# Performance work log

Measured on AMD Instinct MI355X. Metric: run time of the kernel, lower is better.

The kernel has to match this reference:

```python
import jax, jax.numpy as jnp
import numpy as np
import math

NG, NP, NC = 300, 100000, 80
ALPHA, BETA = 0.75, 1.0
K_MAX, K_MIN = 10, 1
EPS = 1e-7


def k_schedule(epoch, total_epochs):
    t = epoch / max(1, total_epochs - 1)
    K = int(round(K_MAX - (K_MAX - K_MIN) * t))
    return max(K_MIN, min(K_MAX, K))


def setup_inputs() -> dict:
    key = jax.random.key(0)
    k1, k2, k3 = jax.random.split(key, 3)
    preds = jax.random.normal(k1, (NP, 5 + NC), dtype=jnp.float32)
    gt_boxes = jax.random.uniform(k2, (NG, 4), dtype=jnp.float32)
    gt_classes = jax.random.randint(k3, (NG,), 0, NC, dtype=jnp.int32)
    return {"preds": preds, "gt_boxes": gt_boxes, "gt_classes": gt_classes,
            "epoch": 0, "total_epochs": 300}


def _cost_matrix(preds, gt_boxes, gt_classes):
    # preds: [Np, 5+C] (xywh, obj, cls_logits); gt_boxes: [Ng, 4] xyxy
    xc, yc, w, h = preds[:, 0], preds[:, 1], preds[:, 2], preds[:, 3]
    p = jnp.stack([xc - w / 2, yc - h / 2, xc + w / 2, yc + h / 2], axis=-1)  # [Np,4] xyxy
    g = gt_boxes  # [Ng,4]

    p_ = p[None, :, :]   # [1,Np,4]
    g_ = g[:, None, :]   # [Ng,1,4]

    # IoU  (bbox_iou with ci=pred, cj=gt)
    x1 = jnp.maximum(p_[..., 0], g_[..., 0])
    y1 = jnp.maximum(p_[..., 1], g_[..., 1])
    x2 = jnp.minimum(p_[..., 2], g_[..., 2])
    y2 = jnp.minimum(p_[..., 3], g_[..., 3])
    inter = jnp.clip(x2 - x1, 0) * jnp.clip(y2 - y1, 0)          # [Ng,Np]
    area_p = jnp.clip(p[:, 2] - p[:, 0], 0) * jnp.clip(p[:, 3] - p[:, 1], 0)   # [Np]
    area_g = jnp.clip(g[:, 2] - g[:, 0], 0) * jnp.clip(g[:, 3] - g[:, 1], 0)   # [Ng]
    union = area_p[None, :] + area_g[:, None] - inter + EPS
    iou = inter / union

    # center distance
    pcx = (p[:, 0] + p[:, 2]) / 2; pcy = (p[:, 1] + p[:, 3]) / 2   # [Np]
    gcx = (g[:, 0] + g[:, 2]) / 2; gcy = (g[:, 1] + g[:, 3]) / 2   # [Ng]
    center_dist2 = (pcx[None, :] - gcx[:, None]) ** 2 + (pcy[None, :] - gcy[:, None]) ** 2

    # enclosing box diagonal
    c_w = jnp.clip(jnp.maximum(p_[..., 2], g_[..., 2]) - jnp.minimum(p_[..., 0], g_[..., 0]), EPS)
    c_h = jnp.clip(jnp.maximum(p_[..., 3], g_[..., 3]) - jnp.minimum(p_[..., 1], g_[..., 1]), EPS)
    c2 = c_w ** 2 + c_h ** 2 + EPS

    # aspect-ratio term
    wp = jnp.clip(p[:, 2] - p[:, 0], EPS); hp = jnp.clip(p[:, 3] - p[:, 1], EPS)  # [Np]
    wg = jnp.clip(g[:, 2] - g[:, 0], EPS); hg = jnp.clip(g[:, 3] - g[:, 1], EPS)  # [Ng]
    v = (4.0 / math.pi ** 2) * (jnp.arctan(wg / hg)[:, None] - jnp.arctan(wp / hp)[None, :]) ** 2
    alpha_t = jax.lax.stop_gradient(v / ((1.0 - iou) + v + EPS))   # torch.no_grad block
    ciou = iou - center_dist2 / c2 - alpha_t * v                   # [Ng,Np] (= 1 - ciou_loss)

    # classification score for each pred at its gt's class
    cls_prob = jax.nn.sigmoid(preds[:, 5:])                        # [Np,C]
    cls_score = jnp.take(cls_prob, gt_classes, axis=1).T           # [Ng,Np]

    cost = ALPHA * (1.0 - cls_score) + BETA * (1.0 - jnp.clip(ciou, 0.0, 1.0))
    return cost


def reference(preds, gt_boxes, gt_classes, epoch, total_epochs):
    Ng, Np = gt_boxes.shape[0], preds.shape[0]
    Kt = min(k_schedule(epoch, total_epochs), Np)
    cost = _cost_matrix(preds, gt_boxes, gt_classes)               # [Ng,Np]
    _, topk_idx = jax.lax.top_k(-cost, Kt)                         # [Ng,Kt] smallest cost per gt
    gt_idx = jnp.broadcast_to(jnp.arange(Ng, dtype=topk_idx.dtype)[:, None], topk_idx.shape)
    assignments = jnp.stack([topk_idx.reshape(-1), gt_idx.reshape(-1)], axis=1)  # [Ng*Kt,2]
    return cost, assignments
```

## Files before the change

kernel.cpp:

```cpp
#include <hip/hip_runtime.h>
#include <math.h>

#define NG 300
#define NP 100000
#define NC 80
#define PRED_COLS 85
#define ALPHA_C 0.75f
#define BETA_C  1.0f
#define EPS_C   1e-7f
#define TPB 256
#define BCH 10
#define CHUNK (NP / BCH)
#define KCAP 10
#define NSLAB 20
#define GSLAB (NG / NSLAB)
#define CTILE 16
#define NCT (NC / CTILE)

__device__ __forceinline__ float fast_rcp(float x) {
    return __builtin_amdgcn_rcpf(x);
}

__global__ __launch_bounds__(TPB) void prep_kernel(
    const float* __restrict__ preds, float* __restrict__ probs,
    float4* __restrict__ bA, float4* __restrict__ bB)
{
    int p = blockIdx.x * TPB + threadIdx.x;
    if (p >= NP) return;
    if (blockIdx.y < NCT) {
        int c0 = blockIdx.y * CTILE;
        const float* row = preds + (size_t)p * PRED_COLS + 5 + c0;
#pragma unroll
        for (int j = 0; j < CTILE; ++j) {
            float l = row[j];
            probs[(size_t)(c0 + j) * NP + p] = fast_rcp(1.f + expf(-l));
        }
    } else {
        const float* row = preds + (size_t)p * PRED_COLS;
        float xc = row[0], yc = row[1], w = row[2], h = row[3];
        float px1 = xc - w * 0.5f, py1 = yc - h * 0.5f;
        float px2 = xc + w * 0.5f, py2 = yc + h * 0.5f;
        float4 a = {px1, py1, px2, py2};
        float4 b;
        b.x = fmaxf(px2 - px1, 0.f) * fmaxf(py2 - py1, 0.f);
        b.y = (px1 + px2) * 0.5f;
        b.z = (py1 + py2) * 0.5f;
        b.w = atanf(fmaxf(px2 - px1, EPS_C) / fmaxf(py2 - py1, EPS_C));
        bA[p] = a; bB[p] = b;
    }
}

template <bool USE_PACK>
__global__ __launch_bounds__(TPB) void cost_kernel(
    const float* __restrict__ preds, const float* __restrict__ gt_boxes,
    const int* __restrict__ gt_classes, float* __restrict__ cost,
    const float* __restrict__ probs,
    const float4* __restrict__ bA, const float4* __restrict__ bB)
{
    __shared__ float4 sbox[GSLAB];
    __shared__ float4 smisc[GSLAB];
    __shared__ int    scls[GSLAB];

    const int g0 = blockIdx.y * GSLAB;

    for (int i = threadIdx.x; i < GSLAB; i += TPB) {
        int g = g0 + i;
        float4 b = ((const float4*)gt_boxes)[g];
        float x1 = b.x, y1 = b.y, x2 = b.z, y2 = b.w;
        sbox[i] = b;
        float4 m;
        m.x = fmaxf(x2 - x1, 0.f) * fmaxf(y2 - y1, 0.f);
        m.y = (x1 + x2) * 0.5f;
        m.z = (y1 + y2) * 0.5f;
        m.w = atanf(fmaxf(x2 - x1, EPS_C) / fmaxf(y2 - y1, EPS_C));
        smisc[i] = m;
        scls[i] = gt_classes[g] * NP;
    }
    __syncthreads();

    int p = blockIdx.x * TPB + threadIdx.x;
    if (p >= NP) return;

    float px1, py1, px2, py2, areap, pcx, pcy, atp;
    if (USE_PACK) {
        float4 a = bA[p], b = bB[p];
        px1 = a.x; py1 = a.y; px2 = a.z; py2 = a.w;
        areap = b.x; pcx = b.y; pcy = b.z; atp = b.w;
    } else {
        const float* row = preds + (size_t)p * PRED_COLS;
        float xc = row[0], yc = row[1], w = row[2], h = row[3];
        px1 = xc - w * 0.5f; py1 = yc - h * 0.5f;
        px2 = xc + w * 0.5f; py2 = yc + h * 0.5f;
        areap = fmaxf(px2 - px1, 0.f) * fmaxf(py2 - py1, 0.f);
        pcx = (px1 + px2) * 0.5f; pcy = (py1 + py2) * 0.5f;
        atp = atanf(fmaxf(px2 - px1, EPS_C) / fmaxf(py2 - py1, EPS_C));
    }

    const float VC = (float)(4.0 / (M_PI * M_PI));
    float* out = cost + (size_t)g0 * NP + p;

#pragma unroll 5
    for (int i = 0; i < GSLAB; ++i) {
        float4 b = sbox[i];
        float4 m = smisc[i];
        float gx1 = b.x, gy1 = b.y, gx2 = b.z, gy2 = b.w;
        float xx1 = fmaxf(px1, gx1), yy1 = fmaxf(py1, gy1);
        float xx2 = fminf(px2, gx2), yy2 = fminf(py2, gy2);
        float inter = fmaxf(xx2 - xx1, 0.f) * fmaxf(yy2 - yy1, 0.f);
        float uni = areap + m.x - inter + EPS_C;
        float iou = inter * fast_rcp(uni);
        float dx = pcx - m.y, dy = pcy - m.z;
        float cd2 = dx * dx + dy * dy;
        float cw = fmaxf(fmaxf(px2, gx2) - fminf(px1, gx1), EPS_C);
        float ch = fmaxf(fmaxf(py2, gy2) - fminf(py1, gy1), EPS_C);
        float c2 = cw * cw + ch * ch + EPS_C;
        float dat = m.w - atp;
        float v = VC * dat * dat;
        float alpha_t = v * fast_rcp(1.f - iou + v + EPS_C);
        float ciou = iou - cd2 * fast_rcp(c2) - alpha_t * v;

        float prob = probs[(size_t)scls[i] + p];
        float cst = ALPHA_C * (1.f - prob) +
                    BETA_C * (1.f - fminf(fmaxf(ciou, 0.f), 1.f));
        out[(size_t)i * NP] = cst;
    }
}

__device__ __forceinline__ void wave_lexmin(float& v, int& i) {
#pragma unroll
    for (int off = 32; off >= 1; off >>= 1) {
        float ov = __shfl_xor(v, off);
        int   oi = __shfl_xor(i, off);
        if (ov < v || (ov == v && oi < i)) { v = ov; i = oi; }
    }
}

__global__ __launch_bounds__(TPB) void topk_partial(
    const float* __restrict__ cost, float* __restrict__ lc, int* __restrict__ li)
{
    int g  = blockIdx.x / BCH;
    int ch = blockIdx.x % BCH;
    const float4* b4 = (const float4*)(cost + (size_t)g * NP + (size_t)ch * CHUNK);
    const int NV = CHUNK / 4;

    const int lane = threadIdx.x & 63;
    const int wid  = threadIdx.x >> 6;

    float lmin = INFINITY;
    for (int i = threadIdx.x; i < NV; i += TPB) {
        float4 v = b4[i];
        lmin = fminf(lmin, fminf(fminf(v.x, v.y), fminf(v.z, v.w)));
    }
    float thr;
    {
        float v = lmin;
        float last = INFINITY;
#pragma unroll
        for (int k = 0; k < KCAP; ++k) {
            float wv = v; int wi = lane;
            wave_lexmin(wv, wi);
            last = wv;
            if (lane == wi) v = INFINITY;
        }
        thr = last;
    }

    float ev = INFINITY;
    int   ei = 0x7fffffff;

    for (int i = threadIdx.x; i < NV; i += TPB) {
        float4 v = b4[i];
        int ib = ch * CHUNK + i * 4;
        float vmin = fminf(fminf(v.x, v.y), fminf(v.z, v.w));
        if (__ballot(vmin <= thr) == 0ull) continue;

        float vq[4] = {v.x, v.y, v.z, v.w};
#pragma unroll
        for (int q = 0; q < 4; ++q) {
            unsigned long long m = __ballot(vq[q] <= thr);
            while (m) {
                int l = __ffsll(m) - 1;
                m &= m - 1;
                float cv = __shfl(vq[q], l);
                int   ci = __shfl(ib, l) + q;
                if (!(cv <= thr)) continue;
                bool prec = (ev < cv) || (ev == cv && ei < ci);
                unsigned long long bb = __ballot(prec) & 0x3FFull;
                int pos = __popcll(bb);
                if (pos < KCAP) {
                    float pev = __shfl_up(ev, 1);
                    int   pei = __shfl_up(ei, 1);
                    if (lane > pos && lane < KCAP) { ev = pev; ei = pei; }
                    if (lane == pos)               { ev = cv;  ei = ci;  }
                    thr = fminf(thr, __shfl(ev, KCAP - 1));
                }
            }
        }
    }

    __shared__ float swv[4 * KCAP];
    __shared__ int   swi[4 * KCAP];
    if (lane < KCAP) { swv[wid * KCAP + lane] = ev; swi[wid * KCAP + lane] = ei; }
    __syncthreads();

    if (wid == 0) {
        float mv = (lane < 4 * KCAP) ? swv[lane] : INFINITY;
        int   mi = (lane < 4 * KCAP) ? swi[lane] : 0x7fffffff;
        float* oc = lc + ((size_t)g * BCH + ch) * KCAP;
        int*   oi = li + ((size_t)g * BCH + ch) * KCAP;
        for (int k = 0; k < KCAP; ++k) {
            float wv = mv; int wi = mi;
            wave_lexmin(wv, wi);
            if (lane == 0) { oc[k] = wv; oi[k] = wi; }
            if (mv == wv && mi == wi) { mv = INFINITY; mi = 0x7fffffff; }
        }
    }
}

__global__ __launch_bounds__(64) void topk_final(
    const float* __restrict__ lc, const int* __restrict__ li,
    const int* __restrict__ epoch, const int* __restrict__ total_epochs,
    float* __restrict__ out_assign)
{
    const int NE = BCH * KCAP;
    int g = blockIdx.x;
    int lane = threadIdx.x;

    float e0 = INFINITY, e1 = INFINITY;
    int   i0 = 0x7fffffff, i1 = 0x7fffffff;
    {
        const float* pc = lc + (size_t)g * NE;
        const int*   pi = li + (size_t)g * NE;
        e0 = pc[lane]; i0 = pi[lane];
        if (lane < NE - 64) { e1 = pc[lane + 64]; i1 = pi[lane + 64]; }
    }

    int ep = epoch[0], te = total_epochs[0];
    int denom = te - 1; if (denom < 1) denom = 1;
    double tt = (double)ep / (double)denom;
    int K = (int)rint(10.0 - 9.0 * tt);
    if (K < 1) K = 1; if (K > 10) K = 10;
    int Kt = (K < NP) ? K : NP;

    for (int k = 0; k < Kt; ++k) {
        bool sel0 = (e0 < e1) || (e0 == e1 && i0 < i1);
        float wv = sel0 ? e0 : e1;
        int   wi = sel0 ? i0 : i1;
        wave_lexmin(wv, wi);
        if (lane == 0) {
            out_assign[2 * ((size_t)g * Kt + k) + 0] = (float)wi;
            out_assign[2 * ((size_t)g * Kt + k) + 1] = (float)g;
        }
        if (e0 == wv && i0 == wi) { e0 = INFINITY; i0 = 0x7fffffff; }
        if (e1 == wv && i1 == wi) { e1 = INFINITY; i1 = 0x7fffffff; }
    }
}

extern "C" void kernel_launch(void* const* d_in, const int* in_sizes, int n_in,
                              void* d_out, int out_size, void* d_ws, size_t ws_size,
                              hipStream_t stream)
{
    const float* preds        = (const float*)d_in[0];
    const float* gt_boxes     = (const float*)d_in[1];
    const int*   gt_classes   = (const int*)d_in[2];
    const int*   epoch        = (const int*)d_in[3];
    const int*   total_epochs = (const int*)d_in[4];

    float* cost       = (float*)d_out;
    float* out_assign = cost + (size_t)NG * NP;

    const int ablocks = (NP + TPB - 1) / TPB;
    size_t probBytes  = (size_t)NC * NP * sizeof(float);
    size_t packBytes  = (size_t)NP * 8 * sizeof(float);
    size_t listBytes  = (size_t)NG * BCH * KCAP * 8;

    char* wsp = (char*)d_ws;
    bool usePack = ws_size >= probBytes + packBytes + listBytes;

    float*  probs = (float*)wsp;
    float4* bA    = (float4*)(wsp + probBytes);
    float4* bB    = (float4*)(wsp + probBytes + packBytes / 2);
    float*  lc; int* li;
    if (usePack) {
        lc = (float*)(wsp + probBytes + packBytes);
        li = (int*)  (wsp + probBytes + packBytes + listBytes / 2);
    } else {
        lc = (float*)(wsp + probBytes);
        li = (int*)  (wsp + probBytes + listBytes / 2);
    }

    if (usePack) {
        prep_kernel<<<dim3(ablocks, NCT + 1), TPB, 0, stream>>>(preds, probs, bA, bB);
        cost_kernel<true ><<<dim3(ablocks, NSLAB), TPB, 0, stream>>>(
            preds, gt_boxes, gt_classes, cost, probs, bA, bB);
    } else {
        prep_kernel<<<dim3(ablocks, NCT), TPB, 0, stream>>>(preds, probs, bA, bB);
        cost_kernel<false><<<dim3(ablocks, NSLAB), TPB, 0, stream>>>(
            preds, gt_boxes, gt_classes, cost, probs, bA, bB);
    }

    topk_partial<<<NG * BCH, TPB, 0, stream>>>(cost, lc, li);
    topk_final<<<NG, 64, 0, stream>>>(lc, li, epoch, total_epochs, out_assign);
}
```

Baseline: 251.2 us.

## Fuse per-block min reduction into cost kernel to precompute top-k thresholds

The cost kernel now computes per-block, per-gt minima while it writes the cost matrix. A new small kernel picks the 10th-smallest of those block minima as a global threshold per gt. topk_partial then skips its own first full pass over the cost matrix, removing one read of the 120 MB cost array. The sigmoid prep is also regrouped into 2 y-blocks, and the probabilities for each slab are hoisted into registers, which adds register pressure and an extra launch.

```diff
diff --git a/kernel.cpp b/kernel.cpp
--- a/kernel.cpp
+++ b/kernel.cpp
@@ -9,16 +9,31 @@
 #define BETA_C  1.0f
 #define EPS_C   1e-7f
 #define TPB 256
+#define NBLK ((NP + TPB - 1) / TPB)
 #define BCH 10
 #define CHUNK (NP / BCH)
 #define KCAP 10
 #define NSLAB 20
 #define GSLAB (NG / NSLAB)
-#define CTILE 16
-#define NCT (NC / CTILE)
 
 __device__ __forceinline__ float fast_rcp(float x) {
     return __builtin_amdgcn_rcpf(x);
+}
+
+__device__ __forceinline__ float wave_min(float v) {
+#pragma unroll
+    for (int off = 32; off >= 1; off >>= 1)
+        v = fminf(v, __shfl_xor(v, off));
+    return v;
+}
+
+__device__ __forceinline__ void wave_lexmin(float& v, int& i) {
+#pragma unroll
+    for (int off = 32; off >= 1; off >>= 1) {
+        float ov = __shfl_xor(v, off);
+        int   oi = __shfl_xor(i, off);
+        if (ov < v || (ov == v && oi < i)) { v = ov; i = oi; }
+    }
 }
 
 __global__ __launch_bounds__(TPB) void prep_kernel(
@@ -27,16 +42,8 @@
 {
     int p = blockIdx.x * TPB + threadIdx.x;
     if (p >= NP) return;
-    if (blockIdx.y < NCT) {
-        int c0 = blockIdx.y * CTILE;
-        const float* row = preds + (size_t)p * PRED_COLS + 5 + c0;
-#pragma unroll
-        for (int j = 0; j < CTILE; ++j) {
-            float l = row[j];
-            probs[(size_t)(c0 + j) * NP + p] = fast_rcp(1.f + expf(-l));
-        }
-    } else {
-        const float* row = preds + (size_t)p * PRED_COLS;
+    const float* row = preds + (size_t)p * PRED_COLS;
+    if (blockIdx.y == 0) {
         float xc = row[0], yc = row[1], w = row[2], h = row[3];
         float px1 = xc - w * 0.5f, py1 = yc - h * 0.5f;
         float px2 = xc + w * 0.5f, py2 = yc + h * 0.5f;
@@ -47,6 +54,13 @@
         b.z = (py1 + py2) * 0.5f;
         b.w = atanf(fmaxf(px2 - px1, EPS_C) / fmaxf(py2 - py1, EPS_C));
         bA[p] = a; bB[p] = b;
+#pragma unroll
+        for (int c = 0; c < 40; ++c)
+            probs[(size_t)c * NP + p] = fast_rcp(1.f + expf(-row[5 + c]));
+    } else {
+#pragma unroll
+        for (int c = 40; c < 80; ++c)
+            probs[(size_t)c * NP + p] = fast_rcp(1.f + expf(-row[5 + c]));
     }
 }
 
@@ -55,13 +69,17 @@
     const float* __restrict__ preds, const float* __restrict__ gt_boxes,
     const int* __restrict__ gt_classes, float* __restrict__ cost,
     const float* __restrict__ probs,
-    const float4* __restrict__ bA, const float4* __restrict__ bB)
+    const float4* __restrict__ bA, const float4* __restrict__ bB,
+    float* __restrict__ mins)
 {
     __shared__ float4 sbox[GSLAB];
     __shared__ float4 smisc[GSLAB];
     __shared__ int    scls[GSLAB];
+    __shared__ float  swmin[4][GSLAB];
 
     const int g0 = blockIdx.y * GSLAB;
+    const int lane = threadIdx.x & 63;
+    const int wid  = threadIdx.x >> 6;
 
     for (int i = threadIdx.x; i < GSLAB; i += TPB) {
         int g = g0 + i;
@@ -74,20 +92,21 @@
         m.z = (y1 + y2) * 0.5f;
         m.w = atanf(fmaxf(x2 - x1, EPS_C) / fmaxf(y2 - y1, EPS_C));
         smisc[i] = m;
-        scls[i] = gt_classes[g] * NP;
+        scls[i] = USE_PACK ? gt_classes[g] * NP : gt_classes[g];
     }
     __syncthreads();
 
-    int p = blockIdx.x * TPB + threadIdx.x;
-    if (p >= NP) return;
+    const int p = blockIdx.x * TPB + threadIdx.x;
+    const bool valid = p < NP;
+    const int pc = valid ? p : NP - 1;
 
     float px1, py1, px2, py2, areap, pcx, pcy, atp;
+    const float* row = preds + (size_t)pc * PRED_COLS;
     if (USE_PACK) {
-        float4 a = bA[p], b = bB[p];
+        float4 a = bA[pc], b = bB[pc];
         px1 = a.x; py1 = a.y; px2 = a.z; py2 = a.w;
         areap = b.x; pcx = b.y; pcy = b.z; atp = b.w;
     } else {
-        const float* row = preds + (size_t)p * PRED_COLS;
         float xc = row[0], yc = row[1], w = row[2], h = row[3];
         px1 = xc - w * 0.5f; py1 = yc - h * 0.5f;
         px2 = xc + w * 0.5f; py2 = yc + h * 0.5f;
@@ -96,10 +115,18 @@
         atp = atanf(fmaxf(px2 - px1, EPS_C) / fmaxf(py2 - py1, EPS_C));
     }
 
+    float prob[GSLAB];
+#pragma unroll
+    for (int i = 0; i < GSLAB; ++i) {
+        if (USE_PACK) prob[i] = probs[(size_t)scls[i] + pc];
+        else          prob[i] = fast_rcp(1.f + expf(-row[5 + scls[i]]));
+    }
+
     const float VC = (float)(4.0 / (M_PI * M_PI));
     float* out = cost + (size_t)g0 * NP + p;
-
-#pragma unroll 5
+    float mn[GSLAB];
+
+#pragma unroll
     for (int i = 0; i < GSLAB; ++i) {
         float4 b = sbox[i];
         float4 m = smisc[i];
@@ -119,24 +146,58 @@
         float alpha_t = v * fast_rcp(1.f - iou + v + EPS_C);
         float ciou = iou - cd2 * fast_rcp(c2) - alpha_t * v;
 
-        float prob = probs[(size_t)scls[i] + p];
-        float cst = ALPHA_C * (1.f - prob) +
+        float cst = ALPHA_C * (1.f - prob[i]) +
                     BETA_C * (1.f - fminf(fmaxf(ciou, 0.f), 1.f));
-        out[(size_t)i * NP] = cst;
-    }
-}
-
-__device__ __forceinline__ void wave_lexmin(float& v, int& i) {
-#pragma unroll
-    for (int off = 32; off >= 1; off >>= 1) {
-        float ov = __shfl_xor(v, off);
-        int   oi = __shfl_xor(i, off);
-        if (ov < v || (ov == v && oi < i)) { v = ov; i = oi; }
-    }
+        mn[i] = valid ? cst : INFINITY;
+        if (valid) out[(size_t)i * NP] = cst;
+    }
+
+#pragma unroll
+    for (int i = 0; i < GSLAB; ++i) {
+        float v = wave_min(mn[i]);
+        if (lane == 0) swmin[wid][i] = v;
+    }
+    __syncthreads();
+    if (threadIdx.x < GSLAB) {
+        int t = threadIdx.x;
+        float v = fminf(fminf(swmin[0][t], swmin[1][t]),
+                        fminf(swmin[2][t], swmin[3][t]));
+        mins[(size_t)(g0 + t) * NBLK + blockIdx.x] = v;
+    }
+}
+
+__global__ __launch_bounds__(64) void thr_kernel(
+    const float* __restrict__ mins, float* __restrict__ thr)
+{
+    int g = blockIdx.x, lane = threadIdx.x;
+    const float* m = mins + (size_t)g * NBLK;
+    float v[7];
+#pragma unroll
+    for (int j = 0; j < 7; ++j) {
+        int idx = lane + j * 64;
+        v[j] = (idx < NBLK) ? m[idx] : INFINITY;
+    }
+    float last = INFINITY;
+    for (int k = 0; k < KCAP; ++k) {
+        float lm = v[0];
+#pragma unroll
+        for (int j = 1; j < 7; ++j) lm = fminf(lm, v[j]);
+        float wv = lm; int wi = lane;
+        wave_lexmin(wv, wi);
+        last = wv;
+        if (lane == wi) {
+            bool done = false;
+#pragma unroll
+            for (int j = 0; j < 7; ++j)
+                if (!done && v[j] == lm) { v[j] = INFINITY; done = true; }
+        }
+    }
+    if (lane == 0) thr[g] = last;
 }
 
 __global__ __launch_bounds__(TPB) void topk_partial(
-    const float* __restrict__ cost, float* __restrict__ lc, int* __restrict__ li)
+    const float* __restrict__ cost, const float* __restrict__ thrbuf,
+    float* __restrict__ lc, int* __restrict__ li)
 {
     int g  = blockIdx.x / BCH;
     int ch = blockIdx.x % BCH;
@@ -146,25 +207,7 @@
     const int lane = threadIdx.x & 63;
     const int wid  = threadIdx.x >> 6;
 
-    float lmin = INFINITY;
-    for (int i = threadIdx.x; i < NV; i += TPB) {
-        float4 v = b4[i];
-        lmin = fminf(lmin, fminf(fminf(v.x, v.y), fminf(v.z, v.w)));
-    }
-    float thr;
-    {
-        float v = lmin;
-        float last = INFINITY;
-#pragma unroll
-        for (int k = 0; k < KCAP; ++k) {
-            float wv = v; int wi = lane;
-            wave_lexmin(wv, wi);
-            last = wv;
-            if (lane == wi) v = INFINITY;
-        }
-        thr = last;
-    }
-
+    float thr = thrbuf[g];
     float ev = INFINITY;
     int   ei = 0x7fffffff;
 
@@ -269,36 +312,41 @@
     float* cost       = (float*)d_out;
     float* out_assign = cost + (size_t)NG * NP;
 
-    const int ablocks = (NP + TPB - 1) / TPB;
-    size_t probBytes  = (size_t)NC * NP * sizeof(float);
-    size_t packBytes  = (size_t)NP * 8 * sizeof(float);
-    size_t listBytes  = (size_t)NG * BCH * KCAP * 8;
+    size_t probBytes = (size_t)NC * NP * sizeof(float);
+    size_t packBytes = (size_t)NP * 8 * sizeof(float);
+    size_t minsBytes = (size_t)NG * NBLK * sizeof(float);
+    size_t thrBytes  = 1216;
+    size_t listBytes = (size_t)NG * BCH * KCAP * 8;
 
     char* wsp = (char*)d_ws;
-    bool usePack = ws_size >= probBytes + packBytes + listBytes;
-
-    float*  probs = (float*)wsp;
-    float4* bA    = (float4*)(wsp + probBytes);
-    float4* bB    = (float4*)(wsp + probBytes + packBytes / 2);
-    float*  lc; int* li;
+    bool usePack = ws_size >= probBytes + packBytes + minsBytes + thrBytes + listBytes;
+
+    float *probs, *minsb, *thrb, *lcb; float4 *bA, *bB; int *lib;
     if (usePack) {
-        lc = (float*)(wsp + probBytes + packBytes);
-        li = (int*)  (wsp + probBytes + packBytes + listBytes / 2);
+        probs = (float*)wsp;
+        bA    = (float4*)(wsp + probBytes);
+        bB    = (float4*)(wsp + probBytes + packBytes / 2);
+        minsb = (float*)(wsp + probBytes + packBytes);
+        thrb  = (float*)(wsp + probBytes + packBytes + minsBytes);
+        lcb   = (float*)(wsp + probBytes + packBytes + minsBytes + thrBytes);
+        lib   = (int*)  (wsp + probBytes + packBytes + minsBytes + thrBytes + listBytes / 2);
     } else {
-        lc = (float*)(wsp + probBytes);
-        li = (int*)  (wsp + probBytes + listBytes / 2);
+        probs = nullptr; bA = nullptr; bB = nullptr;
+        minsb = (float*)wsp;
+        thrb  = (float*)(wsp + minsBytes);
+        lcb   = (float*)(wsp + minsBytes + thrBytes);
+        lib   = (int*)  (wsp + minsBytes + thrBytes + listBytes / 2);
     }
 
     if (usePack) {
-        prep_kernel<<<dim3(ablocks, NCT + 1), TPB, 0, stream>>>(preds, probs, bA, bB);
-        cost_kernel<true ><<<dim3(ablocks, NSLAB), TPB, 0, stream>>>(
-            preds, gt_boxes, gt_classes, cost, probs, bA, bB);
+        prep_kernel<<<dim3(NBLK, 2), TPB, 0, stream>>>(preds, probs, bA, bB);
+        cost_kernel<true ><<<dim3(NBLK, NSLAB), TPB, 0, stream>>>(
+            preds, gt_boxes, gt_classes, cost, probs, bA, bB, minsb);
     } else {
-        prep_kernel<<<dim3(ablocks, NCT), TPB, 0, stream>>>(preds, probs, bA, bB);
-        cost_kernel<false><<<dim3(ablocks, NSLAB), TPB, 0, stream>>>(
-            preds, gt_boxes, gt_classes, cost, probs, bA, bB);
-    }
-
-    topk_partial<<<NG * BCH, TPB, 0, stream>>>(cost, lc, li);
-    topk_final<<<NG, 64, 0, stream>>>(lc, li, epoch, total_epochs, out_assign);
-}
+        cost_kernel<false><<<dim3(NBLK, NSLAB), TPB, 0, stream>>>(
+            preds, gt_boxes, gt_classes, cost, probs, bA, bB, minsb);
+    }
+    thr_kernel<<<NG, 64, 0, stream>>>(minsb, thrb);
+    topk_partial<<<NG * BCH, TPB, 0, stream>>>(cost, thrb, lcb, lib);
+    topk_final<<<NG, 64, 0, stream>>>(lcb, lib, epoch, total_epochs, out_assign);
+}
```

Result: faster. 245.5 us (-2.3%).
